# Performance work log

Hardware: AMD Instinct MI355X
Metric: run time of the kernel (lower is better)

## Reference

```python
import jax, jax.numpy as jnp
import numpy as np
import math

D_MODEL = 1024
NUM_HEADS = 16
HEAD_DIM = D_MODEL // NUM_HEADS
THETA = 10000.0
B, S = 2, 2048


def apply_rope(x, pos, theta=THETA):
    # x: [..., S, D]; pos: [S] int. Rotates consecutive (even, odd) pairs.
    d = x.shape[-1]
    inv_freq = theta ** (-jnp.arange(0, d, 2, dtype=jnp.float32) / d)  # [d/2]
    ang = pos.astype(jnp.float32)[:, None] * inv_freq[None, :]          # [S, d/2]
    cos, sin = jnp.cos(ang), jnp.sin(ang)
    xe = x[..., 0::2]
    xo = x[..., 1::2]
    re = xe * cos - xo * sin
    ro = xe * sin + xo * cos
    return jnp.stack([re, ro], axis=-1).reshape(x.shape)


def setup_inputs() -> dict:
    key = jax.random.key(0)
    ks = jax.random.split(key, 5)
    scale = 1.0 / math.sqrt(D_MODEL)
    return {
        "in_features": jax.random.normal(ks[0], (B, S, D_MODEL), dtype=jnp.float32),
        "token_positions": jnp.arange(S, dtype=jnp.int32),
        "wq": jax.random.normal(ks[1], (D_MODEL, D_MODEL), dtype=jnp.float32) * scale,
        "wk": jax.random.normal(ks[2], (D_MODEL, D_MODEL), dtype=jnp.float32) * scale,
        "wv": jax.random.normal(ks[3], (D_MODEL, D_MODEL), dtype=jnp.float32) * scale,
        "wo": jax.random.normal(ks[4], (D_MODEL, D_MODEL), dtype=jnp.float32) * scale,
    }


def reference(in_features, token_positions, wq, wk, wv, wo):
    x = in_features
    b, s, d = x.shape
    # Linear: y = x @ W.T  (weight stored as [out, in])
    def split_heads(y):
        return y.reshape(b, s, NUM_HEADS, HEAD_DIM).transpose(0, 2, 1, 3)  # [B,H,S,Dh]
    Q = split_heads(x @ wq.T)
    K = split_heads(x @ wk.T)
    V = split_heads(x @ wv.T)
    Q = apply_rope(Q, token_positions)
    K = apply_rope(K, token_positions)
    scores = jnp.einsum('bhqd,bhkd->bhqk', Q, K) / math.sqrt(HEAD_DIM)
    causal = jnp.tril(jnp.ones((s, s), dtype=bool))
    scores = jnp.where(causal, scores, -jnp.inf)
    weights = jax.nn.softmax(scores, axis=-1)
    out = jnp.einsum('bhqk,bhkd->bhqd', weights, V)  # [B,H,S,Dh]
    out = out.transpose(0, 2, 1, 3).reshape(b, s, d)
    return out @ wo.T
```

## Files before the change

### kernel.cpp

```cpp
#include <hip/hip_runtime.h>
#include <hip/hip_bf16.h>

typedef __bf16 bf16_t;
typedef __bf16 bf16x8 __attribute__((ext_vector_type(8)));
typedef __bf16 bf16x4 __attribute__((ext_vector_type(4)));
typedef float  f32x4  __attribute__((ext_vector_type(4)));
typedef float  f32x16 __attribute__((ext_vector_type(16)));
typedef unsigned int u32;
typedef unsigned int u32x2v __attribute__((ext_vector_type(2)));
typedef unsigned int u32x4v __attribute__((ext_vector_type(4)));

#define D_MODEL   1024
#define NQKV      3072
#define NUM_HEADS 16
#define HEAD_DIM  64
#define SEQ       2048
#define BATCH     2
#define NTOK      4096
#define SM_SCALE_LOG2E 0.18033688011112042f
#define LOG2_THETA 13.287712379549449f
#define NEG_BIG  (-3.0e38f)

__device__ __forceinline__ int swz128(int row, int bytecol) {
  return row*128 + ((((bytecol>>4) ^ (row&7))<<4) | (bytecol & 15));
}

__device__ __forceinline__ void gload16(const void* g, void* l) {
  __builtin_amdgcn_global_load_lds((const __attribute__((address_space(1))) u32*)g,
                                   (__attribute__((address_space(3))) u32*)l, 16, 0, 0);
}

__device__ __forceinline__ u32 cvtpk_bf16(float a, float b) {
  u32 r;
  asm("v_cvt_pk_bf16_f32 %0, %1, %2" : "=v"(r) : "v"(a), "v"(b));
  return r;
}

__device__ __forceinline__ void plswap(u32 &a, u32 &b) {
#if __has_builtin(__builtin_amdgcn_permlane32_swap)
  u32x2v r = __builtin_amdgcn_permlane32_swap(a, b, false, false);
  a = r[0]; b = r[1];
#else
  u32 xa = __shfl_xor((unsigned)a, 32, 64);
  u32 xb = __shfl_xor((unsigned)b, 32, 64);
  bool hi = (threadIdx.x & 32) != 0;
  a = hi ? xb : a;
  b = hi ? b : xa;
#endif
}

__device__ const unsigned char slot_order96[96] = {
  30,31,88,90,92,93,94,95,
  28,29,80,82,84,85,86,87,89,91,
  26,27,72,74,76,77,78,79,81,83,
  24,25,64,66,68,69,70,71,73,75,
  22,23,56,58,60,61,62,63,65,67,
  20,21,48,50,52,53,54,55,57,59,
  18,19,40,42,44,45,46,47,49,51,
  16,17,32,34,36,37,38,39,41,43,
  14,15,33,35,
  12,13, 10,11, 8,9, 6,7, 4,5, 2,3, 0,1
};

__global__ void cvt_all(const float* __restrict__ x,  const float* __restrict__ wq,
                        const float* __restrict__ wk, const float* __restrict__ wv,
                        const float* __restrict__ wo,
                        bf16_t* __restrict__ xb, bf16_t* __restrict__ wqkv,
                        bf16_t* __restrict__ wob) {
  const int NX = NTOK*D_MODEL;
  const int NW = D_MODEL*D_MODEL;
  int i = (blockIdx.x*256 + threadIdx.x)*4;
  float4 v; bf16_t* dst;
  if (i < NX) { v = *reinterpret_cast<const float4*>(x + i); dst = xb + i; }
  else {
    int k = i - NX;
    if      (k <   NW) { v = *reinterpret_cast<const float4*>(wq + k);        dst = wqkv + k; }
    else if (k < 2*NW) { v = *reinterpret_cast<const float4*>(wk + k -   NW); dst = wqkv + k; }
    else if (k < 3*NW) { v = *reinterpret_cast<const float4*>(wv + k - 2*NW); dst = wqkv + k; }
    else               { v = *reinterpret_cast<const float4*>(wo + k - 3*NW); dst = wob + k - 3*NW; }
  }
  bf16x4 o; o[0]=(bf16_t)v.x; o[1]=(bf16_t)v.y; o[2]=(bf16_t)v.z; o[3]=(bf16_t)v.w;
  *reinterpret_cast<bf16x4*>(dst) = o;
}

template<typename OutT, bool QKV>
__global__ __launch_bounds__(256, 1) void gemm8(const bf16_t* __restrict__ A,
                                                const bf16_t* __restrict__ B,
                                                OutT* __restrict__ C,
                                                bf16_t* __restrict__ Vt,
                                                const int* __restrict__ pos,
                                                int M, int N, int K) {
  __shared__ __align__(16) char lds[4][32768];
  int tid = threadIdx.x;
  int n0 = blockIdx.x*128, m0 = blockIdx.y*128;
  int wid = tid>>6, lane = tid&63;
  int wr = wid>>1, wc = wid&1;
  int lr = lane&15, lg = lane>>4;

  const int nT = K >> 6;

  int srow = tid >> 3;
  int sc8  = (tid & 7) ^ (srow & 7);
  const bf16_t* ga = A + (size_t)(m0 + srow)*K + sc8*8;
  const bf16_t* gb = B + (size_t)(n0 + srow)*K + sc8*8;

  f32x4 acc[4][4];
  #pragma unroll
  for (int a=0;a<4;a++)
    #pragma unroll
    for (int b=0;b<4;b++) acc[a][b] = (f32x4){0.f,0.f,0.f,0.f};

  auto stage = [&](int t) {
    char* s = lds[t&3];
    int k0 = t << 6;
    #pragma unroll
    for (int g=0; g<4; g++)
      gload16(ga + (size_t)(g*32)*K + k0, s + g*4096 + tid*16);
    #pragma unroll
    for (int g=0; g<4; g++)
      gload16(gb + (size_t)(g*32)*K + k0, s + 16384 + g*4096 + tid*16);
  };

  stage(0);
  if (nT > 1) stage(1);
  asm volatile("s_waitcnt vmcnt(8)" ::: "memory");
  __builtin_amdgcn_sched_barrier(0);
  __builtin_amdgcn_s_barrier();

  for (int t = 0; t < nT; ++t) {
    char* sA = lds[t&3];
    char* sB = sA + 16384;

    bf16x8 bq[4][2], aq[2][2];
    #pragma unroll
    for (int ni=0; ni<4; ni++)
      #pragma unroll
      for (int ks=0; ks<2; ks++)
        bq[ni][ks] = *reinterpret_cast<const bf16x8*>(sB + swz128(wc*64+ni*16+lr, ks*64+lg*16));
    #pragma unroll
    for (int mi=0; mi<2; mi++)
      #pragma unroll
      for (int ks=0; ks<2; ks++)
        aq[mi][ks] = *reinterpret_cast<const bf16x8*>(sA + swz128(wr*64+mi*16+lr, ks*64+lg*16));
    if (t + 2 < nT) stage(t + 2);
    asm volatile("s_waitcnt lgkmcnt(0)" ::: "memory");
    __builtin_amdgcn_sched_barrier(0);
    __builtin_amdgcn_s_setprio(1);
    #pragma unroll
    for (int mi=0; mi<2; mi++)
      #pragma unroll
      for (int ni=0; ni<4; ni++)
        #pragma unroll
        for (int ks=0; ks<2; ks++)
          acc[mi][ni] = __builtin_amdgcn_mfma_f32_16x16x32_bf16(aq[mi][ks], bq[ni][ks], acc[mi][ni], 0, 0, 0);
    __builtin_amdgcn_s_setprio(0);
    __builtin_amdgcn_s_barrier();

    bf16x8 aq2[2][2];
    #pragma unroll
    for (int mi=0; mi<2; mi++)
      #pragma unroll
      for (int ks=0; ks<2; ks++)
        aq2[mi][ks] = *reinterpret_cast<const bf16x8*>(sA + swz128(wr*64+(mi+2)*16+lr, ks*64+lg*16));
    asm volatile("s_waitcnt lgkmcnt(0)" ::: "memory");
    __builtin_amdgcn_sched_barrier(0);
    __builtin_amdgcn_s_setprio(1);
    #pragma unroll
    for (int mi=0; mi<2; mi++)
      #pragma unroll
      for (int ni=0; ni<4; ni++)
        #pragma unroll
        for (int ks=0; ks<2; ks++)
          acc[mi+2][ni] = __builtin_amdgcn_mfma_f32_16x16x32_bf16(aq2[mi][ks], bq[ni][ks], acc[mi+2][ni], 0, 0, 0);
    __builtin_amdgcn_s_setprio(0);
    if (t + 2 < nT)      { asm volatile("s_waitcnt vmcnt(8)" ::: "memory"); }
    else if (t + 1 < nT) { asm volatile("s_waitcnt vmcnt(0)" ::: "memory"); }
    __builtin_amdgcn_sched_barrier(0);
    __builtin_amdgcn_s_barrier();
  }

  if (QKV && n0 < 2*D_MODEL) {
    bool isQ = (n0 < D_MODEL);
    float fr[4];
    #pragma unroll
    for (int ni=0; ni<4; ni++) {
      int j = ((wc*64 + ni*16 + lr) & 63) >> 1;
      fr[ni] = exp2f(-(float)j * (LOG2_THETA/32.0f));
    }
    #pragma unroll
    for (int mi=0; mi<4; mi++)
      #pragma unroll
      for (int r=0; r<4; r++) {
        int m = m0 + wr*64 + mi*16 + lg*4 + r;
        float pt = (float)pos[m & (SEQ-1)];
        #pragma unroll
        for (int ni=0; ni<4; ni++) {
          int n = n0 + wc*64 + ni*16 + lr;
          float v = acc[mi][ni][r];
          float p = __shfl_xor(v, 1, 64);
          float sv, cv;
          __sincosf(pt * fr[ni], &sv, &cv);
          float o = (n & 1) ? (p*sv + v*cv) : (v*cv - p*sv);
          if (isQ) o *= SM_SCALE_LOG2E;
          C[(size_t)m*N + n] = (OutT)o;
        }
      }
  } else if (!QKV) {
    #pragma unroll
    for (int mi=0;mi<4;mi++)
      #pragma unroll
      for (int ni=0;ni<4;ni++)
        #pragma unroll
        for (int r=0;r<4;r++) {
          int m = m0 + wr*64 + mi*16 + lg*4 + r;
          int n = n0 + wc*64 + ni*16 + lr;
          C[(size_t)m*N + n] = (OutT)acc[mi][ni][r];
        }
  } else {
    #pragma unroll
    for (int mi=0;mi<4;mi++)
      #pragma unroll
      for (int ni=0;ni<4;ni++)
        #pragma unroll
        for (int r=0;r<4;r++) {
          int m = m0 + wr*64 + mi*16 + lg*4 + r;
          int nl = n0 + wc*64 + ni*16 + lr - 2*D_MODEL;
          int h = nl >> 6, d = nl & 63;
          int bb = m >> 11, s = m & (SEQ-1);
          Vt[(((size_t)(bb*16 + h)*64 + d) << 11) + s] = (bf16_t)acc[mi][ni][r];
        }
  }
}

__global__ __launch_bounds__(64, 2) void attn9(const bf16_t* __restrict__ QKV,
                                               const bf16_t* __restrict__ Vt,
                                               bf16_t* __restrict__ pO,
                                               float2* __restrict__ pML) {
  __shared__ __align__(16) char sK[64*128];
  __shared__ __align__(16) char sV[64*128];

  int bh = blockIdx.x;
  int b = bh >> 4, h = bh & 15;
  int lane = threadIdx.x & 63;
  int q32 = lane & 31, hi = lane >> 5;
  int rsub = lane >> 3, sg = (lane & 7) ^ rsub;

  int s = slot_order96[blockIdx.y];
  int qw, t0, t1;
  if (s < 32) { qw = s; t0 = 0; t1 = (s >> 1) + 1; }
  else {
    int e = s - 32;
    qw = 32 + (e >> 1);
    int nt = (qw >> 1) + 1, h0 = (nt + 1) >> 1;
    t0 = (e & 1) ? h0 : 0;
    t1 = (e & 1) ? nt : h0;
  }
  int qt   = qw >> 1;
  int slot = bh*96 + s;
  int qg   = qw*32 + q32;

  bf16x8 qf[4];
  const bf16_t* qrow = QKV + (size_t)(b*SEQ + qw*32 + q32)*NQKV + h*64 + hi*8;
  #pragma unroll
  for (int d=0; d<4; d++) qf[d] = *reinterpret_cast<const bf16x8*>(qrow + d*16);

  const bf16_t* kgb = QKV + D_MODEL + ((size_t)(b*SEQ) + rsub)*NQKV + h*64 + sg*8;
  const bf16_t* vgb = Vt + (size_t)bh*64*SEQ + (size_t)rsub*SEQ + sg*8;

  auto stageK = [&](int t) {
    const bf16_t* src = kgb + (size_t)t*64*NQKV;
    #pragma unroll
    for (int c=0;c<8;c++)
      gload16(src + (size_t)(8*c)*NQKV, sK + c*1024 + lane*16);
  };
  auto stageV = [&](int t) {
    const bf16_t* src = vgb + t*64;
    #pragma unroll
    for (int c=0;c<8;c++)
      gload16(src + (size_t)(8*c)*SEQ, sV + c*1024 + lane*16);
  };

  f32x16 O0 = (f32x16)0.0f, O1 = (f32x16)0.0f;
  float mrun = NEG_BIG, lrun = 0.f;

  stageK(t0); stageV(t0);
  asm volatile("s_waitcnt vmcnt(0)" ::: "memory");
  __builtin_amdgcn_sched_barrier(0);

  for (int ti = t0; ti < t1; ++ti) {
    bf16x8 k0f[4], k1f[4], v0f[4], v1f[4];
    #pragma unroll
    for (int ds=0; ds<4; ds++) {
      k0f[ds] = *reinterpret_cast<const bf16x8*>(sK + swz128(q32,    ds*32 + hi*16));
      k1f[ds] = *reinterpret_cast<const bf16x8*>(sK + swz128(32+q32, ds*32 + hi*16));
      v0f[ds] = *reinterpret_cast<const bf16x8*>(sV + swz128(q32,    ds*32 + hi*16));
      v1f[ds] = *reinterpret_cast<const bf16x8*>(sV + swz128(32+q32, ds*32 + hi*16));
    }
    asm volatile("s_waitcnt lgkmcnt(0)" ::: "memory");
    __builtin_amdgcn_sched_barrier(0);
    if (ti + 1 < t1) { stageK(ti + 1); stageV(ti + 1); }

    f32x16 p0 = (f32x16)0.0f, p1 = (f32x16)0.0f;
    __builtin_amdgcn_s_setprio(1);
    #pragma unroll
    for (int ds=0; ds<4; ds++) {
      p0 = __builtin_amdgcn_mfma_f32_32x32x16_bf16(k0f[ds], qf[ds], p0, 0, 0, 0);
      p1 = __builtin_amdgcn_mfma_f32_32x32x16_bf16(k1f[ds], qf[ds], p1, 0, 0, 0);
    }
    __builtin_amdgcn_s_setprio(0);

    if (ti == qt) {
      #pragma unroll
      for (int r=0; r<16; r++) {
        int kg = ti*64 + (r&3) + 8*(r>>2) + 4*hi;
        if (kg      > qg) p0[r] = NEG_BIG;
        if (kg + 32 > qg) p1[r] = NEG_BIG;
      }
    }

    float mx[8];
    #pragma unroll
    for (int r=0;r<8;r++) mx[r] = fmaxf(fmaxf(p0[r],p0[r+8]), fmaxf(p1[r],p1[r+8]));
    #pragma unroll
    for (int st=4; st>0; st>>=1)
      #pragma unroll
      for (int r=0;r<st;r++) mx[r] = fmaxf(mx[r], mx[r+st]);
    float mt   = fmaxf(mx[0], __shfl_xor(mx[0], 32, 64));
    float mnew = fmaxf(mrun, mt);
    float alpha = exp2f(mrun - mnew);
    #pragma unroll
    for (int r=0; r<16; r++) {
      p0[r] = exp2f(p0[r] - mnew);
      p1[r] = exp2f(p1[r] - mnew);
    }
    float sx[8];
    #pragma unroll
    for (int r=0;r<8;r++) sx[r] = (p0[r]+p0[r+8]) + (p1[r]+p1[r+8]);
    #pragma unroll
    for (int st=4; st>0; st>>=1)
      #pragma unroll
      for (int r=0;r<st;r++) sx[r] += sx[r+st];
    float stot = sx[0] + __shfl_xor(sx[0], 32, 64);
    lrun = lrun*alpha + stot;
    mrun = mnew;
    O0 *= alpha; O1 *= alpha;

    u32 pk0[8], pk1[8];
    #pragma unroll
    for (int i2=0; i2<8; i2++) {
      pk0[i2] = cvtpk_bf16(p0[2*i2], p0[2*i2+1]);
      pk1[i2] = cvtpk_bf16(p1[2*i2], p1[2*i2+1]);
    }
    plswap(pk0[0], pk0[2]); plswap(pk0[1], pk0[3]);
    plswap(pk0[4], pk0[6]); plswap(pk0[5], pk0[7]);
    plswap(pk1[0], pk1[2]); plswap(pk1[1], pk1[3]);
    plswap(pk1[4], pk1[6]); plswap(pk1[5], pk1[7]);

    bf16x8 pa[4];
    pa[0] = __builtin_bit_cast(bf16x8, (u32x4v){pk0[0],pk0[1],pk0[2],pk0[3]});
    pa[1] = __builtin_bit_cast(bf16x8, (u32x4v){pk0[4],pk0[5],pk0[6],pk0[7]});
    pa[2] = __builtin_bit_cast(bf16x8, (u32x4v){pk1[0],pk1[1],pk1[2],pk1[3]});
    pa[3] = __builtin_bit_cast(bf16x8, (u32x4v){pk1[4],pk1[5],pk1[6],pk1[7]});

    __builtin_amdgcn_s_setprio(1);
    #pragma unroll
    for (int ks=0; ks<4; ks++) {
      O0 = __builtin_amdgcn_mfma_f32_32x32x16_bf16(v0f[ks], pa[ks], O0, 0, 0, 0);
      O1 = __builtin_amdgcn_mfma_f32_32x32x16_bf16(v1f[ks], pa[ks], O1, 0, 0, 0);
    }
    __builtin_amdgcn_s_setprio(0);

    if (ti + 1 < t1) {
      asm volatile("s_waitcnt vmcnt(0)" ::: "memory");
      __builtin_amdgcn_sched_barrier(0);
    }
  }

  bf16_t* prow = pO + ((size_t)slot*2048 + q32*64);
  #pragma unroll
  for (int rg=0; rg<4; rg++) {
    int d0 = 8*rg + 4*hi;
    u32 a0 = cvtpk_bf16(O0[4*rg],   O0[4*rg+1]);
    u32 a1 = cvtpk_bf16(O0[4*rg+2], O0[4*rg+3]);
    *reinterpret_cast<u32x2v*>(prow + d0) = (u32x2v){a0, a1};
    u32 b0 = cvtpk_bf16(O1[4*rg],   O1[4*rg+1]);
    u32 b1 = cvtpk_bf16(O1[4*rg+2], O1[4*rg+3]);
    *reinterpret_cast<u32x2v*>(prow + 32 + d0) = (u32x2v){b0, b1};
  }
  if (hi == 0)
    pML[slot*32 + q32] = make_float2(mrun, lrun);
}

__global__ __launch_bounds__(128) void combine(const bf16_t* __restrict__ pO,
                                               const float2* __restrict__ pML,
                                               bf16_t* __restrict__ Of) {
  int qw = blockIdx.x, bh = blockIdx.y;
  int b = bh >> 4, h = bh & 15;
  int t = threadIdx.x;
  int q = t >> 2, d0 = (t & 3) * 16;
  bf16x8 r0, r1;
  if (qw < 32) {
    int slot = bh*96 + qw;
    float2 ml = pML[slot*32 + q];
    float inv = 1.0f / ml.y;
    const bf16x8* src = reinterpret_cast<const bf16x8*>(pO + (size_t)slot*2048 + q*64 + d0);
    bf16x8 o0 = src[0], o1 = src[1];
    #pragma unroll
    for (int i=0;i<8;i++) {
      r0[i] = (bf16_t)((float)o0[i]*inv);
      r1[i] = (bf16_t)((float)o1[i]*inv);
    }
  } else {
    int s0 = bh*96 + 32 + (qw-32)*2;
    float2 mlA = pML[s0*32 + q];
    float2 mlB = pML[(s0+1)*32 + q];
    float m  = fmaxf(mlA.x, mlB.x);
    float a0 = exp2f(mlA.x - m), a1 = exp2f(mlB.x - m);
    float inv = 1.0f / (a0*mlA.y + a1*mlB.y);
    a0 *= inv; a1 *= inv;
    const bf16x8* sA = reinterpret_cast<const bf16x8*>(pO + (size_t)s0*2048 + q*64 + d0);
    const bf16x8* sB = reinterpret_cast<const bf16x8*>(pO + (size_t)(s0+1)*2048 + q*64 + d0);
    bf16x8 oa0 = sA[0], oa1 = sA[1], ob0 = sB[0], ob1 = sB[1];
    #pragma unroll
    for (int i=0;i<8;i++) {
      r0[i] = (bf16_t)(a0*(float)oa0[i] + a1*(float)ob0[i]);
      r1[i] = (bf16_t)(a0*(float)oa1[i] + a1*(float)ob1[i]);
    }
  }
  bf16x8* dst = reinterpret_cast<bf16x8*>(Of + ((size_t)(b*SEQ) + qw*32 + q)*D_MODEL + h*64 + d0);
  dst[0] = r0; dst[1] = r1;
}

extern "C" void kernel_launch(void* const* d_in, const int* in_sizes, int n_in,
                              void* d_out, int out_size, void* d_ws, size_t ws_size,
                              hipStream_t stream) {
  const float* x   = (const float*)d_in[0];
  const int*   pos = (const int*)  d_in[1];
  const float* wq  = (const float*)d_in[2];
  const float* wk  = (const float*)d_in[3];
  const float* wv  = (const float*)d_in[4];
  const float* wo  = (const float*)d_in[5];
  float* out = (float*)d_out;

  char* ws = (char*)d_ws;
  bf16_t* xb   = (bf16_t*)(ws);
  bf16_t* wqkv = (bf16_t*)(ws + ( 8u<<20));
  bf16_t* wob  = (bf16_t*)(ws + (14u<<20));
  bf16_t* QKV  = (bf16_t*)(ws + (16u<<20));
  bf16_t* Vtb  = (bf16_t*)(ws + (40u<<20));
  bf16_t* pO   = (bf16_t*)(ws);
  float2* pML  = (float2*)(ws + (13u<<20));
  bf16_t* Of   = (bf16_t*)(ws + (40u<<20));

  cvt_all<<<8*D_MODEL*D_MODEL/1024, 256, 0, stream>>>(x, wq, wk, wv, wo, xb, wqkv, wob);

  dim3 gqkv(NQKV/128, NTOK/128);
  gemm8<bf16_t, true><<<gqkv, 256, 0, stream>>>(xb, wqkv, QKV, Vtb, pos, NTOK, NQKV, D_MODEL);

  dim3 gattn(32, 96);
  attn9<<<gattn, 64, 0, stream>>>(QKV, Vtb, pO, pML);

  dim3 gcomb(64, 32);
  combine<<<gcomb, 128, 0, stream>>>(pO, pML, Of);

  dim3 gout(D_MODEL/128, NTOK/128);
  gemm8<float, false><<<gout, 256, 0, stream>>>(Of, wob, out, nullptr, nullptr, NTOK, D_MODEL, D_MODEL);
}
```

Measured before the change: 125.5 us.

## Split long causal query tiles four ways and add lazy softmax rescaling

Attention work is split more finely. Query tiles 0-15 are handled unsplit, tiles 16-47 are split in two along the key range, and tiles 48-63 in four, giving 144 work slots per head ordered longest-first. This balances load across CUs better. The combine kernel now merges up to four partial results. The QK buffer is shrunk to a 2048-wide layout with V stored only transposed, and the partial-output buffers are reorganised in the workspace. The online softmax now skips the rescale of O and l unless the new max exceeds the running max by more than 8 (log2 units). This cuts per-tile ALU work but relies on fp32 headroom for values up to 2^8.

```diff
diff --git a/kernel.cpp b/kernel.cpp
--- a/kernel.cpp
+++ b/kernel.cpp
@@ -12,6 +12,7 @@
 
 #define D_MODEL   1024
 #define NQKV      3072
+#define NQK       2048
 #define NUM_HEADS 16
 #define HEAD_DIM  64
 #define SEQ       2048
@@ -49,17 +50,20 @@
 #endif
 }
 
-__device__ const unsigned char slot_order96[96] = {
-  30,31,88,90,92,93,94,95,
-  28,29,80,82,84,85,86,87,89,91,
-  26,27,72,74,76,77,78,79,81,83,
-  24,25,64,66,68,69,70,71,73,75,
-  22,23,56,58,60,61,62,63,65,67,
-  20,21,48,50,52,53,54,55,57,59,
-  18,19,40,42,44,45,46,47,49,51,
-  16,17,32,34,36,37,38,39,41,43,
-  14,15,33,35,
-  12,13, 10,11, 8,9, 6,7, 4,5, 2,3, 0,1
+__device__ const unsigned char slot_order144[144] = {
+  72,74,76,77,78,79,
+  64,66,68,69,70,71,73,75,
+  56,58,60,61,62,63,65,67,
+  48,50,52,53,54,55,57,59,
+  14,15,40,42,44,45,46,47,49,51,115,119,121,123,125,127,129,130,131,133,
+  134,135,136,137,138,139,140,141,142,143,
+  12,13,32,34,36,37,38,39,41,43,83,87,89,91,93,95,97,98,99,101,
+  102,103,104,105,106,107,108,109,110,111,112,113,114,116,117,118,120,122,124,126,
+  128,132,
+  10,11,24,26,28,29,30,31,33,35,80,81,82,84,85,86,88,90,92,94,96,100,
+  8,9,16,18,20,21,22,23,25,27,
+  6,7,17,19,
+  4,5, 2,3, 0,1
 };
 
 __global__ void cvt_all(const float* __restrict__ x,  const float* __restrict__ wq,
@@ -98,6 +102,7 @@
   int lr = lane&15, lg = lane>>4;
 
   const int nT = K >> 6;
+  const int CN = QKV ? NQK : N;
 
   int srow = tid >> 3;
   int sc8  = (tid & 7) ^ (srow & 7);
@@ -202,7 +207,7 @@
           __sincosf(pt * fr[ni], &sv, &cv);
           float o = (n & 1) ? (p*sv + v*cv) : (v*cv - p*sv);
           if (isQ) o *= SM_SCALE_LOG2E;
-          C[(size_t)m*N + n] = (OutT)o;
+          C[(size_t)m*CN + n] = (OutT)o;
         }
       }
   } else if (!QKV) {
@@ -214,7 +219,7 @@
         for (int r=0;r<4;r++) {
           int m = m0 + wr*64 + mi*16 + lg*4 + r;
           int n = n0 + wc*64 + ni*16 + lr;
-          C[(size_t)m*N + n] = (OutT)acc[mi][ni][r];
+          C[(size_t)m*CN + n] = (OutT)acc[mi][ni][r];
         }
   } else {
     #pragma unroll
@@ -232,10 +237,11 @@
   }
 }
 
-__global__ __launch_bounds__(64, 2) void attn9(const bf16_t* __restrict__ QKV,
-                                               const bf16_t* __restrict__ Vt,
-                                               bf16_t* __restrict__ pO,
-                                               float2* __restrict__ pML) {
+__global__ __launch_bounds__(64, 2) void attn14(const bf16_t* __restrict__ QK,
+                                                const bf16_t* __restrict__ Vt,
+                                                bf16_t* __restrict__ pOA,
+                                                bf16_t* __restrict__ pOB,
+                                                float2* __restrict__ pML) {
   __shared__ __align__(16) char sK[64*128];
   __shared__ __align__(16) char sV[64*128];
 
@@ -245,33 +251,38 @@
   int q32 = lane & 31, hi = lane >> 5;
   int rsub = lane >> 3, sg = (lane & 7) ^ rsub;
 
-  int s = slot_order96[blockIdx.y];
+  int s = slot_order144[blockIdx.y];
   int qw, t0, t1;
-  if (s < 32) { qw = s; t0 = 0; t1 = (s >> 1) + 1; }
-  else {
-    int e = s - 32;
-    qw = 32 + (e >> 1);
+  if (s < 16) { qw = s; t0 = 0; t1 = (s >> 1) + 1; }
+  else if (s < 80) {
+    int e = s - 16;
+    qw = 16 + (e >> 1);
     int nt = (qw >> 1) + 1, h0 = (nt + 1) >> 1;
     t0 = (e & 1) ? h0 : 0;
     t1 = (e & 1) ? nt : h0;
-  }
-  int qt   = qw >> 1;
-  int slot = bh*96 + s;
-  int qg   = qw*32 + q32;
+  } else {
+    int e = s - 80;
+    qw = 48 + (e >> 2);
+    int nt = (qw >> 1) + 1, qq = e & 3;
+    t0 = (nt * qq) >> 2;
+    t1 = (nt * (qq + 1)) >> 2;
+  }
+  int qt = qw >> 1;
+  int qg = qw*32 + q32;
 
   bf16x8 qf[4];
-  const bf16_t* qrow = QKV + (size_t)(b*SEQ + qw*32 + q32)*NQKV + h*64 + hi*8;
+  const bf16_t* qrow = QK + (size_t)(b*SEQ + qw*32 + q32)*NQK + h*64 + hi*8;
   #pragma unroll
   for (int d=0; d<4; d++) qf[d] = *reinterpret_cast<const bf16x8*>(qrow + d*16);
 
-  const bf16_t* kgb = QKV + D_MODEL + ((size_t)(b*SEQ) + rsub)*NQKV + h*64 + sg*8;
+  const bf16_t* kgb = QK + D_MODEL + ((size_t)(b*SEQ) + rsub)*NQK + h*64 + sg*8;
   const bf16_t* vgb = Vt + (size_t)bh*64*SEQ + (size_t)rsub*SEQ + sg*8;
 
   auto stageK = [&](int t) {
-    const bf16_t* src = kgb + (size_t)t*64*NQKV;
+    const bf16_t* src = kgb + (size_t)t*64*NQK;
     #pragma unroll
     for (int c=0;c<8;c++)
-      gload16(src + (size_t)(8*c)*NQKV, sK + c*1024 + lane*16);
+      gload16(src + (size_t)(8*c)*NQK, sK + c*1024 + lane*16);
   };
   auto stageV = [&](int t) {
     const bf16_t* src = vgb + t*64;
@@ -325,13 +336,19 @@
     for (int st=4; st>0; st>>=1)
       #pragma unroll
       for (int r=0;r<st;r++) mx[r] = fmaxf(mx[r], mx[r+st]);
-    float mt   = fmaxf(mx[0], __shfl_xor(mx[0], 32, 64));
-    float mnew = fmaxf(mrun, mt);
-    float alpha = exp2f(mrun - mnew);
+    float mt = fmaxf(mx[0], __shfl_xor(mx[0], 32, 64));
+
+    if (!__all(mt <= mrun + 8.0f)) {
+      float mnew  = fmaxf(mrun, mt);
+      float alpha = exp2f(mrun - mnew);
+      lrun *= alpha;
+      O0 *= alpha; O1 *= alpha;
+      mrun = mnew;
+    }
     #pragma unroll
     for (int r=0; r<16; r++) {
-      p0[r] = exp2f(p0[r] - mnew);
-      p1[r] = exp2f(p1[r] - mnew);
+      p0[r] = exp2f(p0[r] - mrun);
+      p1[r] = exp2f(p1[r] - mrun);
     }
     float sx[8];
     #pragma unroll
@@ -340,10 +357,7 @@
     for (int st=4; st>0; st>>=1)
       #pragma unroll
       for (int r=0;r<st;r++) sx[r] += sx[r+st];
-    float stot = sx[0] + __shfl_xor(sx[0], 32, 64);
-    lrun = lrun*alpha + stot;
-    mrun = mnew;
-    O0 *= alpha; O1 *= alpha;
+    lrun += sx[0] + __shfl_xor(sx[0], 32, 64);
 
     u32 pk0[8], pk1[8];
     #pragma unroll
@@ -376,7 +390,9 @@
     }
   }
 
-  bf16_t* prow = pO + ((size_t)slot*2048 + q32*64);
+  bf16_t* base = (s < 112) ? (pOA + (size_t)(s*32 + bh)*2048)
+                           : (pOB + (size_t)((s-112)*32 + bh)*2048);
+  bf16_t* prow = base + q32*64;
   #pragma unroll
   for (int rg=0; rg<4; rg++) {
     int d0 = 8*rg + 4*hi;
@@ -388,47 +404,57 @@
     *reinterpret_cast<u32x2v*>(prow + 32 + d0) = (u32x2v){b0, b1};
   }
   if (hi == 0)
-    pML[slot*32 + q32] = make_float2(mrun, lrun);
-}
-
-__global__ __launch_bounds__(128) void combine(const bf16_t* __restrict__ pO,
+    pML[(s*32 + bh)*32 + q32] = make_float2(mrun, lrun);
+}
+
+__global__ __launch_bounds__(128) void combine(const bf16_t* __restrict__ pOA,
+                                               const bf16_t* __restrict__ pOB,
                                                const float2* __restrict__ pML,
                                                bf16_t* __restrict__ Of) {
   int qw = blockIdx.x, bh = blockIdx.y;
   int b = bh >> 4, h = bh & 15;
   int t = threadIdx.x;
   int q = t >> 2, d0 = (t & 3) * 16;
-  bf16x8 r0, r1;
-  if (qw < 32) {
-    int slot = bh*96 + qw;
-    float2 ml = pML[slot*32 + q];
-    float inv = 1.0f / ml.y;
-    const bf16x8* src = reinterpret_cast<const bf16x8*>(pO + (size_t)slot*2048 + q*64 + d0);
-    bf16x8 o0 = src[0], o1 = src[1];
-    #pragma unroll
-    for (int i=0;i<8;i++) {
-      r0[i] = (bf16_t)((float)o0[i]*inv);
-      r1[i] = (bf16_t)((float)o1[i]*inv);
-    }
-  } else {
-    int s0 = bh*96 + 32 + (qw-32)*2;
-    float2 mlA = pML[s0*32 + q];
-    float2 mlB = pML[(s0+1)*32 + q];
-    float m  = fmaxf(mlA.x, mlB.x);
-    float a0 = exp2f(mlA.x - m), a1 = exp2f(mlB.x - m);
-    float inv = 1.0f / (a0*mlA.y + a1*mlB.y);
-    a0 *= inv; a1 *= inv;
-    const bf16x8* sA = reinterpret_cast<const bf16x8*>(pO + (size_t)s0*2048 + q*64 + d0);
-    const bf16x8* sB = reinterpret_cast<const bf16x8*>(pO + (size_t)(s0+1)*2048 + q*64 + d0);
-    bf16x8 oa0 = sA[0], oa1 = sA[1], ob0 = sB[0], ob1 = sB[1];
-    #pragma unroll
-    for (int i=0;i<8;i++) {
-      r0[i] = (bf16_t)(a0*(float)oa0[i] + a1*(float)ob0[i]);
-      r1[i] = (bf16_t)(a0*(float)oa1[i] + a1*(float)ob1[i]);
-    }
-  }
+
+  auto slotp = [&](int s) -> const bf16x8* {
+    const bf16_t* base = (s < 112) ? (pOA + (size_t)(s*32 + bh)*2048)
+                                   : (pOB + (size_t)((s-112)*32 + bh)*2048);
+    return reinterpret_cast<const bf16x8*>(base + q*64 + d0);
+  };
+  auto mlv = [&](int s) -> float2 { return pML[(s*32 + bh)*32 + q]; };
+
+  float r0[8], r1[8];
+  #pragma unroll
+  for (int i=0;i<8;i++) { r0[i]=0.f; r1[i]=0.f; }
+
+  int s0, np;
+  if (qw < 16)      { s0 = qw;               np = 1; }
+  else if (qw < 48) { s0 = 16 + (qw-16)*2;   np = 2; }
+  else              { s0 = 80 + (qw-48)*4;   np = 4; }
+
+  float m = NEG_BIG;
+  float2 ml[4];
+  for (int i=0;i<np;i++) { ml[i] = mlv(s0+i); m = fmaxf(m, ml[i].x); }
+  float lsum = 0.f, w[4];
+  for (int i=0;i<np;i++) { w[i] = exp2f(ml[i].x - m); lsum += w[i]*ml[i].y; }
+  float inv = 1.0f / lsum;
+
+  for (int i=0;i<np;i++) {
+    const bf16x8* sp = slotp(s0+i);
+    bf16x8 o0 = sp[0], o1 = sp[1];
+    float wi = w[i]*inv;
+    #pragma unroll
+    for (int j=0;j<8;j++) {
+      r0[j] += wi*(float)o0[j];
+      r1[j] += wi*(float)o1[j];
+    }
+  }
+
+  bf16x8 y0, y1;
+  #pragma unroll
+  for (int j=0;j<8;j++) { y0[j]=(bf16_t)r0[j]; y1[j]=(bf16_t)r1[j]; }
   bf16x8* dst = reinterpret_cast<bf16x8*>(Of + ((size_t)(b*SEQ) + qw*32 + q)*D_MODEL + h*64 + d0);
-  dst[0] = r0; dst[1] = r1;
+  dst[0] = y0; dst[1] = y1;
 }
 
 extern "C" void kernel_launch(void* const* d_in, const int* in_sizes, int n_in,
@@ -446,22 +472,23 @@
   bf16_t* xb   = (bf16_t*)(ws);
   bf16_t* wqkv = (bf16_t*)(ws + ( 8u<<20));
   bf16_t* wob  = (bf16_t*)(ws + (14u<<20));
-  bf16_t* QKV  = (bf16_t*)(ws + (16u<<20));
+  bf16_t* QK   = (bf16_t*)(ws + (16u<<20));
   bf16_t* Vtb  = (bf16_t*)(ws + (40u<<20));
-  bf16_t* pO   = (bf16_t*)(ws);
-  float2* pML  = (float2*)(ws + (13u<<20));
-  bf16_t* Of   = (bf16_t*)(ws + (40u<<20));
+  bf16_t* pOA  = (bf16_t*)(ws);
+  bf16_t* pOB  = (bf16_t*)(ws + (32u<<20));
+  float2* pML  = (float2*)(ws + (36u<<20));
+  bf16_t* Of   = (bf16_t*)(ws + (16u<<20));
 
   cvt_all<<<8*D_MODEL*D_MODEL/1024, 256, 0, stream>>>(x, wq, wk, wv, wo, xb, wqkv, wob);
 
   dim3 gqkv(NQKV/128, NTOK/128);
-  gemm8<bf16_t, true><<<gqkv, 256, 0, stream>>>(xb, wqkv, QKV, Vtb, pos, NTOK, NQKV, D_MODEL);
-
-  dim3 gattn(32, 96);
-  attn9<<<gattn, 64, 0, stream>>>(QKV, Vtb, pO, pML);
+  gemm8<bf16_t, true><<<gqkv, 256, 0, stream>>>(xb, wqkv, QK, Vtb, pos, NTOK, NQKV, D_MODEL);
+
+  dim3 gattn(32, 144);
+  attn14<<<gattn, 64, 0, stream>>>(QK, Vtb, pOA, pOB, pML);
 
   dim3 gcomb(64, 32);
-  combine<<<gcomb, 128, 0, stream>>>(pO, pML, Of);
+  combine<<<gcomb, 128, 0, stream>>>(pOA, pOB, pML, Of);
 
   dim3 gout(D_MODEL/128, NTOK/128);
   gemm8<float, false><<<gout, 256, 0, stream>>>(Of, wob, out, nullptr, nullptr, NTOK, D_MODEL, D_MODEL);
```

Result: slower. 135.0 us (+7.6%).
